# Kernel optimization log

Hardware: AMD Instinct MI355X
Metric: run time of the kernel (lower is better)

## Reference

```python
import jax, jax.numpy as jnp
import numpy as np

R = 8
TOP_K_A = 2
TOP_K_B = 2
SCALING = 16.0 / R  # lora_alpha / r


def setup_inputs() -> dict:
    key = jax.random.key(0)
    k1, k2, k3, k4, k5 = jax.random.split(key, 5)
    B, S, D_IN, D_OUT, EA, EB = 4, 2048, 4096, 4096, 8, 8
    x = jax.random.normal(k1, (B, S, D_IN), dtype=jnp.float32)
    router_logits_a = jax.random.normal(k2, (B * S, EA), dtype=jnp.float32)
    router_logits_b = jax.random.normal(k3, (B * S, EB), dtype=jnp.float32)
    # nn.Linear(in, r).weight -> [r, in]; stacked per expert: [E_a, r, in]
    Wa = jax.random.normal(k4, (EA, R, D_IN), dtype=jnp.float32) * (1.0 / np.sqrt(D_IN))
    # nn.Linear(r, out).weight -> [out, r]; stacked: [E_b, out, r]
    Wb = jax.random.normal(k5, (EB, D_OUT, R), dtype=jnp.float32) * (1.0 / np.sqrt(R))
    return {"x": x, "router_logits_a": router_logits_a,
            "router_logits_b": router_logits_b, "Wa": Wa, "Wb": Wb}


def reference(x, router_logits_a, router_logits_b, Wa, Wb):
    B, S, D_IN = x.shape
    flat_x = x.reshape(-1, D_IN)  # [T, D_in]

    # --- A experts: dense compute over all experts, then top-k gather ---
    topk_logits_a, topk_idx_a = jax.lax.top_k(router_logits_a, TOP_K_A)
    weights_a = jax.nn.softmax(topk_logits_a, axis=-1)  # [T, k_a]
    a_all = jnp.einsum('ti,eri->ter', flat_x, Wa)  # [T, E_a, r]
    sel_a = jnp.take_along_axis(a_all, topk_idx_a[:, :, None], axis=1)  # [T, k_a, r]
    mid = jnp.sum(sel_a * weights_a[:, :, None], axis=1)  # [T, r]

    # --- B experts: dense compute over all experts, then top-k gather ---
    b_all = jnp.einsum('tr,eor->teo', mid, Wb)  # [T, E_b, D_out]
    topk_logits_b, topk_idx_b = jax.lax.top_k(router_logits_b, TOP_K_B)
    weights_b = jax.nn.softmax(topk_logits_b, axis=-1)  # [T, k_b]
    sel_b = jnp.take_along_axis(b_all, topk_idx_b[:, :, None], axis=1)  # [T, k_b, D_out]
    out_flat = jnp.sum(sel_b * weights_b[:, :, None], axis=1) * SCALING  # [T, D_out]
    output = out_flat.reshape(B, S, -1)

    # --- load-balancing aux losses (torch.var is unbiased) ---
    probs_a = jnp.mean(jax.nn.softmax(router_logits_a, axis=-1), axis=0)
    probs_b = jnp.mean(jax.nn.softmax(router_logits_b, axis=-1), axis=0)
    aux_loss_a = Wa.shape[0] * jnp.var(probs_a, ddof=1)
    aux_loss_b = Wb.shape[0] * jnp.var(probs_b, ddof=1)
    return output, aux_loss_a, aux_loss_b
```

## Files before the change

kernel.cpp:

```cpp
#include <hip/hip_runtime.h>
#include <hip/hip_bf16.h>

#define T_TOK 8192
#define D_IN  4096
#define D_OUT 4096
#define SCALE 2.0f

typedef _Float16 h2 __attribute__((ext_vector_type(2)));
typedef _Float16 h4 __attribute__((ext_vector_type(4)));
typedef _Float16 h8 __attribute__((ext_vector_type(8)));
typedef float    f4v __attribute__((ext_vector_type(4)));

__device__ __forceinline__ h2 pkrtz(float a, float b) {
    auto r = __builtin_amdgcn_cvt_pkrtz(a, b);
    h2 o; __builtin_memcpy(&o, &r, 4); return o;
}


__global__ void cwa(const float* __restrict__ Wa, _Float16* __restrict__ WaB) {
    int gid = blockIdx.x * 256 + threadIdx.x;
    int er  = gid >> 10;
    int k0  = (gid & 1023) * 4;
    float4 v = ((const float4*)Wa)[gid];
    int hoff = ((k0 >> 3) * 64 + er) * 8 + (k0 & 7);
    h2 p0 = pkrtz(v.x, v.y), p1 = pkrtz(v.z, v.w);
    h4 o = { p0.x, p0.y, p1.x, p1.y };
    *(h4*)(WaB + hoff) = o;
}

__global__ void cwb(const float* __restrict__ Wb, _Float16* __restrict__ WbB) {
    int gid = blockIdx.x * 256 + threadIdx.x;
    int o = gid & 4095, er = gid >> 12;
    int e = er >> 3, r = er & 7;
    float v = Wb[((size_t)e * 4096 + o) * 8 + r];
    int nt = o >> 8, nl = o & 255;
    WbB[(size_t)nt * 16384 + ((er >> 3) * 256 + nl) * 8 + (er & 7)] = (_Float16)v;
}

__global__ __launch_bounds__(256)
void g1(const float* __restrict__ x, const _Float16* __restrict__ WaB,
        float* __restrict__ part, int kch) {
    __shared__ _Float16 lA[16 * 33 * 8];
    __shared__ _Float16 lB[16 * 64 * 8];
    const int tx = threadIdx.x, l = tx & 63, w = tx >> 6;
    const int m0 = blockIdx.x * 32;
    const int kb = blockIdx.y * kch;
    const int mf = w >> 1, nh = w & 1;

    f4v acc[2];
    acc[0] = (f4v){0.f, 0.f, 0.f, 0.f};
    acc[1] = (f4v){0.f, 0.f, 0.f, 0.f};

    const int iters = kch >> 7;
    for (int it = 0; it < iters; ++it) {
        __syncthreads();
        const float4* xg = (const float4*)(x + (size_t)m0 * D_IN + kb + it * 128);
#pragma unroll
        for (int i = 0; i < 4; ++i) {
            int f = i * 256 + tx;
            int row = f >> 5, c4 = f & 31;
            float4 v = xg[row * 1024 + c4];
            int k = c4 * 4;
            h2 p0 = pkrtz(v.x, v.y), p1 = pkrtz(v.z, v.w);
            h4 o = { p0.x, p0.y, p1.x, p1.y };
            *(h4*)(lA + ((k >> 3) * 33 + row) * 8 + (k & 7)) = o;
        }
        const uint4* bg = (const uint4*)(WaB + (((size_t)kb + it * 128) >> 3) * 512);
        uint4* lb4 = (uint4*)lB;
#pragma unroll
        for (int i = 0; i < 4; ++i) lb4[i * 256 + tx] = bg[i * 256 + tx];
        __syncthreads();

#pragma unroll
        for (int ks = 0; ks < 4; ++ks) {
            h8 a = *(const h8*)(lA + ((ks * 4 + (l >> 4)) * 33 + mf * 16 + (l & 15)) * 8);
#pragma unroll
            for (int n2 = 0; n2 < 2; ++n2) {
                int nf = nh * 2 + n2;
                h8 b = *(const h8*)(lB + ((ks * 4 + (l >> 4)) * 64 + nf * 16 + (l & 15)) * 8);
                acc[n2] = __builtin_amdgcn_mfma_f32_16x16x32_f16(a, b, acc[n2], 0, 0, 0);
            }
        }
    }
    float* pp = part + (size_t)blockIdx.y * T_TOK * 64;
#pragma unroll
    for (int n2 = 0; n2 < 2; ++n2)
#pragma unroll
        for (int r = 0; r < 4; ++r)
            pp[(size_t)(m0 + mf * 16 + (l >> 4) * 4 + r) * 64
               + nh * 32 + n2 * 16 + (l & 15)] = acc[n2][r];
}

__global__ __launch_bounds__(256)
void comb(const float* __restrict__ part, const float* __restrict__ la,
          const float* __restrict__ lb, _Float16* __restrict__ Mb, int ksplit) {
    const int tx = threadIdx.x, l = tx & 63;
    const int t = blockIdx.x * 4 + (tx >> 6);

    float lg[8];
#pragma unroll
    for (int i = 0; i < 8; ++i) lg[i] = la[t * 8 + i];
    int ea0 = 0; float b0 = lg[0];
#pragma unroll
    for (int i = 1; i < 8; ++i) if (lg[i] > b0) { b0 = lg[i]; ea0 = i; }
    int ea1 = -1; float b1 = -1e30f;
#pragma unroll
    for (int i = 0; i < 8; ++i) if (i != ea0 && lg[i] > b1) { b1 = lg[i]; ea1 = i; }
    float wa1 = __expf(b1 - b0); float sa = 1.0f + wa1;
    float wa0 = 1.0f / sa; wa1 = wa1 / sa;

#pragma unroll
    for (int i = 0; i < 8; ++i) lg[i] = lb[t * 8 + i];
    int f0 = 0; float c0 = lg[0];
#pragma unroll
    for (int i = 1; i < 8; ++i) if (lg[i] > c0) { c0 = lg[i]; f0 = i; }
    int f1 = -1; float c1 = -1e30f;
#pragma unroll
    for (int i = 0; i < 8; ++i) if (i != f0 && lg[i] > c1) { c1 = lg[i]; f1 = i; }
    float wb1 = __expf(c1 - c0); float sb = 1.0f + wb1;
    float wb0 = 1.0f / sb; wb1 = wb1 / sb;

    float s = 0.f;
    for (int c = 0; c < ksplit; ++c) s += part[((size_t)c * T_TOK + t) * 64 + l];

    float a0 = __shfl(s, ea0 * 8 + (l & 7), 64);
    float a1 = __shfl(s, ea1 * 8 + (l & 7), 64);
    float mid = wa0 * a0 + wa1 * a1;
    int e = l >> 3;
    float coef = (e == f0) ? SCALE * wb0 : (e == f1) ? SCALE * wb1 : 0.0f;
    Mb[(size_t)(t >> 6) * 4096 + ((l >> 3) * 64 + (t & 63)) * 8 + (l & 7)]
        = (_Float16)(coef * mid);
}

__global__ __launch_bounds__(256)
void g2(const _Float16* __restrict__ Mb, const _Float16* __restrict__ WbB,
        float* __restrict__ out) {
    __shared__ _Float16 lA[4096];
    __shared__ _Float16 lB[16384];
    const int tx = threadIdx.x, l = tx & 63, w = tx >> 6;
    const int nt = blockIdx.x;
    const int mt = blockIdx.y;

    {   const uint4* g = (const uint4*)(Mb + (size_t)mt * 4096);
        uint4* d = (uint4*)lA;
        d[tx] = g[tx]; d[256 + tx] = g[256 + tx]; }
    {   const uint4* g = (const uint4*)(WbB + (size_t)nt * 16384);
        uint4* d = (uint4*)lB;
#pragma unroll
        for (int j = 0; j < 8; ++j) d[j * 256 + tx] = g[j * 256 + tx]; }
    __syncthreads();

    f4v acc[4][4];
#pragma unroll
    for (int mf = 0; mf < 4; ++mf)
#pragma unroll
        for (int nf = 0; nf < 4; ++nf) acc[mf][nf] = (f4v){0.f, 0.f, 0.f, 0.f};

#pragma unroll
    for (int ks = 0; ks < 2; ++ks) {
        h8 a[4], b[4];
#pragma unroll
        for (int mf = 0; mf < 4; ++mf)
            a[mf] = *(const h8*)(lA + ((ks * 4 + (l >> 4)) * 64 + mf * 16 + (l & 15)) * 8);
#pragma unroll
        for (int nf = 0; nf < 4; ++nf)
            b[nf] = *(const h8*)(lB + ((ks * 4 + (l >> 4)) * 256 + w * 64 + nf * 16 + (l & 15)) * 8);
#pragma unroll
        for (int mf = 0; mf < 4; ++mf)
#pragma unroll
            for (int nf = 0; nf < 4; ++nf)
                acc[mf][nf] = __builtin_amdgcn_mfma_f32_16x16x32_f16(a[mf], b[nf], acc[mf][nf], 0, 0, 0);
    }

#pragma unroll
    for (int mf = 0; mf < 4; ++mf)
#pragma unroll
        for (int nf = 0; nf < 4; ++nf)
#pragma unroll
            for (int r = 0; r < 4; ++r)
                out[(size_t)(mt * 64 + mf * 16 + (l >> 4) * 4 + r) * D_OUT
                    + nt * 256 + w * 64 + nf * 16 + (l & 15)] = acc[mf][nf][r];
}

__global__ void aux_partial(const float* __restrict__ la, const float* __restrict__ lb,
                            double* __restrict__ part) {
    const int tx = threadIdx.x;
    const int t  = blockIdx.x * 256 + tx;
    double loc[16];
    {
        float l[8];
#pragma unroll
        for (int i = 0; i < 8; ++i) l[i] = la[t * 8 + i];
        float m = l[0];
#pragma unroll
        for (int i = 1; i < 8; ++i) m = fmaxf(m, l[i]);
        float s = 0.f; float e[8];
#pragma unroll
        for (int i = 0; i < 8; ++i) { e[i] = __expf(l[i] - m); s += e[i]; }
#pragma unroll
        for (int i = 0; i < 8; ++i) loc[i] = (double)(e[i] / s);
    }
    {
        float l[8];
#pragma unroll
        for (int i = 0; i < 8; ++i) l[i] = lb[t * 8 + i];
        float m = l[0];
#pragma unroll
        for (int i = 1; i < 8; ++i) m = fmaxf(m, l[i]);
        float s = 0.f; float e[8];
#pragma unroll
        for (int i = 0; i < 8; ++i) { e[i] = __expf(l[i] - m); s += e[i]; }
#pragma unroll
        for (int i = 0; i < 8; ++i) loc[8 + i] = (double)(e[i] / s);
    }
    __shared__ double red[4][16];
    const int lane = tx & 63, wid = tx >> 6;
#pragma unroll
    for (int v = 0; v < 16; ++v) {
        double s = loc[v];
#pragma unroll
        for (int off = 32; off > 0; off >>= 1) s += __shfl_down(s, off, 64);
        if (lane == 0) red[wid][v] = s;
    }
    __syncthreads();
    if (tx < 16)
        part[blockIdx.x * 16 + tx] = red[0][tx] + red[1][tx] + red[2][tx] + red[3][tx];
}

__global__ void aux_final(const double* __restrict__ part, float* __restrict__ out_aux) {
    const int tx = threadIdx.x;
    __shared__ double sl[16];
    if (tx < 16) {
        double s = 0.0;
#pragma unroll
        for (int b = 0; b < 32; ++b) s += part[b * 16 + tx];
        sl[tx] = s;
    }
    __syncthreads();
    if (tx == 0) {
        double pa[8], pb[8], ma = 0.0, mb = 0.0;
        for (int e = 0; e < 8; ++e) { pa[e] = sl[e] / 8192.0;     ma += pa[e] / 8.0; }
        for (int e = 0; e < 8; ++e) { pb[e] = sl[8 + e] / 8192.0; mb += pb[e] / 8.0; }
        double va = 0.0, vb = 0.0;
        for (int e = 0; e < 8; ++e) { double d = pa[e] - ma; va += d * d; }
        for (int e = 0; e < 8; ++e) { double d = pb[e] - mb; vb += d * d; }
        va /= 7.0; vb /= 7.0;
        out_aux[0] = (float)(8.0 * va);
        out_aux[1] = (float)(8.0 * vb);
    }
}

extern "C" void kernel_launch(void* const* d_in, const int* in_sizes, int n_in,
                              void* d_out, int out_size, void* d_ws, size_t ws_size,
                              hipStream_t stream) {
    const float* x  = (const float*)d_in[0];
    const float* la = (const float*)d_in[1];
    const float* lb = (const float*)d_in[2];
    const float* Wa = (const float*)d_in[3];
    const float* Wb = (const float*)d_in[4];
    float* out = (float*)d_out;

    char* ws = (char*)d_ws;
    _Float16* WaB = (_Float16*)ws;
    _Float16* WbB = (_Float16*)(ws + 524288);
    _Float16* Mb  = (_Float16*)(ws + 1048576);
    double*   pax = (double*)(ws + 2097152);
    float*    p1  = (float*)(ws + 2162688);

    const size_t base = 2162688;
    int ksplit = (ws_size >= base + 4u * 2097152u) ? 4
               : (ws_size >= base + 2u * 2097152u) ? 2 : 1;
    int kch = D_IN / ksplit;

    cwa<<<256, 256, 0, stream>>>(Wa, WaB);
    cwb<<<1024, 256, 0, stream>>>(Wb, WbB);
    aux_partial<<<32, 256, 0, stream>>>(la, lb, pax);
    g1<<<dim3(256, ksplit), 256, 0, stream>>>(x, WaB, p1, kch);
    comb<<<2048, 256, 0, stream>>>(p1, la, lb, Mb, ksplit);
    g2<<<dim3(16, 128), 256, 0, stream>>>(Mb, WbB, out);
    aux_final<<<1, 64, 0, stream>>>(pax, out + (size_t)T_TOK * D_OUT);
}
```

Baseline: 274.0 us.

## Fuse both LoRA GEMMs, routing combine and aux finalize into one kernel

Merges the two weight-conversion kernels and the aux partial reduction into a single prep launch. A single fused kernel then handles each 16-token tile end to end: the x·Wa GEMM with register double-buffered global loads and no K-split, the top-k routing combine in LDS, and the rank-8 GEMM that writes the output directly. This removes the partial-sum and Mb round trips through global memory and cuts the launch count from seven to two. In exchange, Wb is re-read by every block (512 blocks), and the first GEMM loses the K-split parallelism, so each block runs a long serial K loop.

```diff
diff --git a/kernel.cpp b/kernel.cpp
--- a/kernel.cpp
+++ b/kernel.cpp
@@ -1,10 +1,8 @@
 #include <hip/hip_runtime.h>
-#include <hip/hip_bf16.h>
 
 #define T_TOK 8192
 #define D_IN  4096
 #define D_OUT 4096
-#define SCALE 2.0f
 
 typedef _Float16 h2 __attribute__((ext_vector_type(2)));
 typedef _Float16 h4 __attribute__((ext_vector_type(4)));
@@ -15,238 +13,230 @@
     auto r = __builtin_amdgcn_cvt_pkrtz(a, b);
     h2 o; __builtin_memcpy(&o, &r, 4); return o;
 }
-
-
-__global__ void cwa(const float* __restrict__ Wa, _Float16* __restrict__ WaB) {
-    int gid = blockIdx.x * 256 + threadIdx.x;
-    int er  = gid >> 10;
-    int k0  = (gid & 1023) * 4;
-    float4 v = ((const float4*)Wa)[gid];
-    int hoff = ((k0 >> 3) * 64 + er) * 8 + (k0 & 7);
-    h2 p0 = pkrtz(v.x, v.y), p1 = pkrtz(v.z, v.w);
-    h4 o = { p0.x, p0.y, p1.x, p1.y };
-    *(h4*)(WaB + hoff) = o;
-}
-
-__global__ void cwb(const float* __restrict__ Wb, _Float16* __restrict__ WbB) {
-    int gid = blockIdx.x * 256 + threadIdx.x;
-    int o = gid & 4095, er = gid >> 12;
-    int e = er >> 3, r = er & 7;
-    float v = Wb[((size_t)e * 4096 + o) * 8 + r];
-    int nt = o >> 8, nl = o & 255;
-    WbB[(size_t)nt * 16384 + ((er >> 3) * 256 + nl) * 8 + (er & 7)] = (_Float16)v;
-}
+__device__ __forceinline__ h8 cvt8(float4 f0, float4 f1) {
+    h2 p0 = pkrtz(f0.x, f0.y), p1 = pkrtz(f0.z, f0.w);
+    h2 p2 = pkrtz(f1.x, f1.y), p3 = pkrtz(f1.z, f1.w);
+    return (h8){p0.x, p0.y, p1.x, p1.y, p2.x, p2.y, p3.x, p3.y};
+}
+__device__ __forceinline__ h8 as_h8(uint4 u) { h8 b; __builtin_memcpy(&b, &u, 16); return b; }
+
 
 __global__ __launch_bounds__(256)
-void g1(const float* __restrict__ x, const _Float16* __restrict__ WaB,
-        float* __restrict__ part, int kch) {
-    __shared__ _Float16 lA[16 * 33 * 8];
-    __shared__ _Float16 lB[16 * 64 * 8];
+void prep(const float* __restrict__ Wa, const float* __restrict__ Wb,
+          const float* __restrict__ la, const float* __restrict__ lb,
+          _Float16* __restrict__ WaB, _Float16* __restrict__ WbB,
+          double* __restrict__ pax) {
+    const int bid = blockIdx.x, tx = threadIdx.x;
+    __shared__ double red[4][16];
+    if (bid < 256) {
+        int gid = bid * 256 + tx;
+        int er = gid >> 10, k0 = (gid & 1023) * 4;
+        float4 v = ((const float4*)Wa)[gid];
+        h2 p0 = pkrtz(v.x, v.y), p1 = pkrtz(v.z, v.w);
+        h4 o = { p0.x, p0.y, p1.x, p1.y };
+        *(h4*)(WaB + ((k0 >> 3) * 64 + er) * 8 + (k0 & 7)) = o;
+    } else if (bid < 384) {
+        int gid = (bid - 256) * 256 + tx;
+        int e = gid >> 12, o = gid & 4095;
+        const float4* p = (const float4*)(Wb + ((size_t)e * 4096 + o) * 8);
+        h8 v = cvt8(p[0], p[1]);
+        *(h8*)(WbB + ((size_t)e * 4096 + o) * 8) = v;
+    } else {
+        const int ab = bid - 384;
+        const int t = ab * 256 + tx;
+        double loc[16];
+        {
+            float l[8];
+#pragma unroll
+            for (int i = 0; i < 8; ++i) l[i] = la[(size_t)t * 8 + i];
+            float m = l[0];
+#pragma unroll
+            for (int i = 1; i < 8; ++i) m = fmaxf(m, l[i]);
+            float s = 0.f, e[8];
+#pragma unroll
+            for (int i = 0; i < 8; ++i) { e[i] = __expf(l[i] - m); s += e[i]; }
+#pragma unroll
+            for (int i = 0; i < 8; ++i) loc[i] = (double)(e[i] / s);
+        }
+        {
+            float l[8];
+#pragma unroll
+            for (int i = 0; i < 8; ++i) l[i] = lb[(size_t)t * 8 + i];
+            float m = l[0];
+#pragma unroll
+            for (int i = 1; i < 8; ++i) m = fmaxf(m, l[i]);
+            float s = 0.f, e[8];
+#pragma unroll
+            for (int i = 0; i < 8; ++i) { e[i] = __expf(l[i] - m); s += e[i]; }
+#pragma unroll
+            for (int i = 0; i < 8; ++i) loc[8 + i] = (double)(e[i] / s);
+        }
+        const int lane = tx & 63, wid = tx >> 6;
+#pragma unroll
+        for (int v = 0; v < 16; ++v) {
+            double s = loc[v];
+#pragma unroll
+            for (int off = 32; off > 0; off >>= 1) s += __shfl_down(s, off, 64);
+            if (lane == 0) red[wid][v] = s;
+        }
+        __syncthreads();
+        if (tx < 16)
+            pax[ab * 16 + tx] = red[0][tx] + red[1][tx] + red[2][tx] + red[3][tx];
+    }
+}
+
+__global__ __launch_bounds__(256)
+void fused(const float* __restrict__ x, const _Float16* __restrict__ WaB,
+           const _Float16* __restrict__ WbB, const float* __restrict__ la,
+           const float* __restrict__ lb, float* __restrict__ out,
+           const double* __restrict__ pax) {
+    __shared__ float    pL[16][66];
+    __shared__ _Float16 MbL[1024];
+    __shared__ float    sW0[16], sW1[16], sCb[16][8];
+    __shared__ int      sE0[16], sE1[16];
+    __shared__ double   sl[16];
+
     const int tx = threadIdx.x, l = tx & 63, w = tx >> 6;
-    const int m0 = blockIdx.x * 32;
-    const int kb = blockIdx.y * kch;
-    const int mf = w >> 1, nh = w & 1;
-
-    f4v acc[2];
-    acc[0] = (f4v){0.f, 0.f, 0.f, 0.f};
-    acc[1] = (f4v){0.f, 0.f, 0.f, 0.f};
-
-    const int iters = kch >> 7;
-    for (int it = 0; it < iters; ++it) {
+    const int mr = l & 15, kf = l >> 4;
+    const int m0 = blockIdx.x * 16;
+    const int er1 = w * 16 + mr;
+
+    f4v acc = (f4v){0.f, 0.f, 0.f, 0.f};
+    const float* xr = x + (size_t)(m0 + mr) * D_IN + kf * 8;
+    const uint4* wa4 = (const uint4*)WaB;
+
+    float4 A0[8], A1[8]; uint4 B0[4], B1[4];
+
+#define LD1(Ad, Bd, IT) do {                                                   \
+    const float* ap_ = xr + (IT) * 128;                                        \
+    _Pragma("unroll") for (int ks_ = 0; ks_ < 4; ++ks_) {                      \
+        Ad[2 * ks_]     = *(const float4*)(ap_ + ks_ * 32);                    \
+        Ad[2 * ks_ + 1] = *(const float4*)(ap_ + ks_ * 32 + 4); }              \
+    _Pragma("unroll") for (int ks_ = 0; ks_ < 4; ++ks_)                        \
+        Bd[ks_] = wa4[(size_t)(((IT) * 16 + ks_ * 4 + kf) * 64) + er1];        \
+  } while (0)
+
+#define CMP1(As, Bs) do {                                                      \
+    _Pragma("unroll") for (int ks_ = 0; ks_ < 4; ++ks_) {                      \
+        h8 a_ = cvt8(As[2 * ks_], As[2 * ks_ + 1]);                            \
+        acc = __builtin_amdgcn_mfma_f32_16x16x32_f16(a_, as_h8(Bs[ks_]), acc,  \
+                                                     0, 0, 0); }               \
+  } while (0)
+
+    LD1(A0, B0, 0);
+#pragma unroll 1
+    for (int it = 0; it < 30; it += 2) {
+        LD1(A1, B1, it + 1); CMP1(A0, B0);
+        LD1(A0, B0, it + 2); CMP1(A1, B1);
+    }
+    LD1(A1, B1, 31); CMP1(A0, B0); CMP1(A1, B1);
+#undef LD1
+#undef CMP1
+
+#pragma unroll
+    for (int r = 0; r < 4; ++r) pL[kf * 4 + r][er1] = acc[r];
+    __syncthreads();
+
+    if (tx < 16) {
+        const int t = tx;
+        float lg[8];
+#pragma unroll
+        for (int i = 0; i < 8; ++i) lg[i] = la[(size_t)(m0 + t) * 8 + i];
+        int e0 = 0; float b0 = lg[0];
+#pragma unroll
+        for (int i = 1; i < 8; ++i) if (lg[i] > b0) { b0 = lg[i]; e0 = i; }
+        int e1 = -1; float b1 = -1e30f;
+#pragma unroll
+        for (int i = 0; i < 8; ++i) if (i != e0 && lg[i] > b1) { b1 = lg[i]; e1 = i; }
+        float w1 = __expf(b1 - b0), s = 1.f + w1;
+        sW0[t] = 1.f / s; sW1[t] = w1 / s; sE0[t] = e0; sE1[t] = e1;
+
+#pragma unroll
+        for (int i = 0; i < 8; ++i) lg[i] = lb[(size_t)(m0 + t) * 8 + i];
+        int f0 = 0; float c0 = lg[0];
+#pragma unroll
+        for (int i = 1; i < 8; ++i) if (lg[i] > c0) { c0 = lg[i]; f0 = i; }
+        int f1 = -1; float c1 = -1e30f;
+#pragma unroll
+        for (int i = 0; i < 8; ++i) if (i != f0 && lg[i] > c1) { c1 = lg[i]; f1 = i; }
+        float wb1 = __expf(c1 - c0), sb = 1.f + wb1;
+        float wb0s = 2.f / sb, wb1s = 2.f * wb1 / sb;
+#pragma unroll
+        for (int e = 0; e < 8; ++e)
+            sCb[t][e] = (e == f0) ? wb0s : (e == f1) ? wb1s : 0.f;
+    }
+    __syncthreads();
+
+    {
+        const int t = tx >> 4, g = tx & 15;
+        const float w0 = sW0[t], w1 = sW1[t];
+        const int e0 = sE0[t], e1 = sE1[t];
+        const float cb = sCb[t][g >> 1];
+        h4 o;
+#pragma unroll
+        for (int j = 0; j < 4; ++j) {
+            int r = (g * 4 + j) & 7;
+            float mid = w0 * pL[t][e0 * 8 + r] + w1 * pL[t][e1 * 8 + r];
+            o[j] = (_Float16)(cb * mid);
+        }
+        *(h4*)(MbL + ((g >> 1) * 16 + t) * 8 + (g & 1) * 4) = o;
+    }
+    __syncthreads();
+
+    h8 a30, a31;
+    a30 = *(const h8*)(MbL + ((0 * 4 + kf) * 16 + mr) * 8);
+    a31 = *(const h8*)(MbL + ((1 * 4 + kf) * 16 + mr) * 8);
+    const uint4* wb4 = (const uint4*)WbB;
+    const size_t bofs0 = (size_t)((0 * 4 + kf) * 4096);
+    const size_t bofs1 = (size_t)((1 * 4 + kf) * 4096);
+    float* outp = out + (size_t)(m0 + kf * 4) * D_OUT;
+
+    uint4 C0[4], C1[4];
+#define LDB3(Cd, CH) do { int n0_ = (CH) * 128 + w * 32 + mr;                  \
+    Cd[0] = wb4[bofs0 + n0_];      Cd[1] = wb4[bofs0 + n0_ + 16];              \
+    Cd[2] = wb4[bofs1 + n0_];      Cd[3] = wb4[bofs1 + n0_ + 16];              \
+  } while (0)
+
+#define CMP3(Cs, CH) do {                                                      \
+    f4v o0 = (f4v){0.f,0.f,0.f,0.f}, o1 = (f4v){0.f,0.f,0.f,0.f};              \
+    o0 = __builtin_amdgcn_mfma_f32_16x16x32_f16(a30, as_h8(Cs[0]), o0, 0,0,0); \
+    o0 = __builtin_amdgcn_mfma_f32_16x16x32_f16(a31, as_h8(Cs[2]), o0, 0,0,0); \
+    o1 = __builtin_amdgcn_mfma_f32_16x16x32_f16(a30, as_h8(Cs[1]), o1, 0,0,0); \
+    o1 = __builtin_amdgcn_mfma_f32_16x16x32_f16(a31, as_h8(Cs[3]), o1, 0,0,0); \
+    int n0_ = (CH) * 128 + w * 32 + mr;                                        \
+    _Pragma("unroll") for (int r_ = 0; r_ < 4; ++r_) {                         \
+        outp[(size_t)r_ * D_OUT + n0_]      = o0[r_];                          \
+        outp[(size_t)r_ * D_OUT + n0_ + 16] = o1[r_]; }                        \
+  } while (0)
+
+    LDB3(C0, 0);
+#pragma unroll 1
+    for (int c = 0; c < 30; c += 2) {
+        LDB3(C1, c + 1); CMP3(C0, c);
+        LDB3(C0, c + 2); CMP3(C1, c + 1);
+    }
+    LDB3(C1, 31); CMP3(C0, 30); CMP3(C1, 31);
+#undef LDB3
+#undef CMP3
+
+    if (blockIdx.x == 0) {
+        if (tx < 16) {
+            double s = 0.0;
+#pragma unroll
+            for (int b = 0; b < 32; ++b) s += pax[b * 16 + tx];
+            sl[tx] = s;
+        }
         __syncthreads();
-        const float4* xg = (const float4*)(x + (size_t)m0 * D_IN + kb + it * 128);
-#pragma unroll
-        for (int i = 0; i < 4; ++i) {
-            int f = i * 256 + tx;
-            int row = f >> 5, c4 = f & 31;
-            float4 v = xg[row * 1024 + c4];
-            int k = c4 * 4;
-            h2 p0 = pkrtz(v.x, v.y), p1 = pkrtz(v.z, v.w);
-            h4 o = { p0.x, p0.y, p1.x, p1.y };
-            *(h4*)(lA + ((k >> 3) * 33 + row) * 8 + (k & 7)) = o;
-        }
-        const uint4* bg = (const uint4*)(WaB + (((size_t)kb + it * 128) >> 3) * 512);
-        uint4* lb4 = (uint4*)lB;
-#pragma unroll
-        for (int i = 0; i < 4; ++i) lb4[i * 256 + tx] = bg[i * 256 + tx];
-        __syncthreads();
-
-#pragma unroll
-        for (int ks = 0; ks < 4; ++ks) {
-            h8 a = *(const h8*)(lA + ((ks * 4 + (l >> 4)) * 33 + mf * 16 + (l & 15)) * 8);
-#pragma unroll
-            for (int n2 = 0; n2 < 2; ++n2) {
-                int nf = nh * 2 + n2;
-                h8 b = *(const h8*)(lB + ((ks * 4 + (l >> 4)) * 64 + nf * 16 + (l & 15)) * 8);
-                acc[n2] = __builtin_amdgcn_mfma_f32_16x16x32_f16(a, b, acc[n2], 0, 0, 0);
-            }
-        }
-    }
-    float* pp = part + (size_t)blockIdx.y * T_TOK * 64;
-#pragma unroll
-    for (int n2 = 0; n2 < 2; ++n2)
-#pragma unroll
-        for (int r = 0; r < 4; ++r)
-            pp[(size_t)(m0 + mf * 16 + (l >> 4) * 4 + r) * 64
-               + nh * 32 + n2 * 16 + (l & 15)] = acc[n2][r];
-}
-
-__global__ __launch_bounds__(256)
-void comb(const float* __restrict__ part, const float* __restrict__ la,
-          const float* __restrict__ lb, _Float16* __restrict__ Mb, int ksplit) {
-    const int tx = threadIdx.x, l = tx & 63;
-    const int t = blockIdx.x * 4 + (tx >> 6);
-
-    float lg[8];
-#pragma unroll
-    for (int i = 0; i < 8; ++i) lg[i] = la[t * 8 + i];
-    int ea0 = 0; float b0 = lg[0];
-#pragma unroll
-    for (int i = 1; i < 8; ++i) if (lg[i] > b0) { b0 = lg[i]; ea0 = i; }
-    int ea1 = -1; float b1 = -1e30f;
-#pragma unroll
-    for (int i = 0; i < 8; ++i) if (i != ea0 && lg[i] > b1) { b1 = lg[i]; ea1 = i; }
-    float wa1 = __expf(b1 - b0); float sa = 1.0f + wa1;
-    float wa0 = 1.0f / sa; wa1 = wa1 / sa;
-
-#pragma unroll
-    for (int i = 0; i < 8; ++i) lg[i] = lb[t * 8 + i];
-    int f0 = 0; float c0 = lg[0];
-#pragma unroll
-    for (int i = 1; i < 8; ++i) if (lg[i] > c0) { c0 = lg[i]; f0 = i; }
-    int f1 = -1; float c1 = -1e30f;
-#pragma unroll
-    for (int i = 0; i < 8; ++i) if (i != f0 && lg[i] > c1) { c1 = lg[i]; f1 = i; }
-    float wb1 = __expf(c1 - c0); float sb = 1.0f + wb1;
-    float wb0 = 1.0f / sb; wb1 = wb1 / sb;
-
-    float s = 0.f;
-    for (int c = 0; c < ksplit; ++c) s += part[((size_t)c * T_TOK + t) * 64 + l];
-
-    float a0 = __shfl(s, ea0 * 8 + (l & 7), 64);
-    float a1 = __shfl(s, ea1 * 8 + (l & 7), 64);
-    float mid = wa0 * a0 + wa1 * a1;
-    int e = l >> 3;
-    float coef = (e == f0) ? SCALE * wb0 : (e == f1) ? SCALE * wb1 : 0.0f;
-    Mb[(size_t)(t >> 6) * 4096 + ((l >> 3) * 64 + (t & 63)) * 8 + (l & 7)]
-        = (_Float16)(coef * mid);
-}
-
-__global__ __launch_bounds__(256)
-void g2(const _Float16* __restrict__ Mb, const _Float16* __restrict__ WbB,
-        float* __restrict__ out) {
-    __shared__ _Float16 lA[4096];
-    __shared__ _Float16 lB[16384];
-    const int tx = threadIdx.x, l = tx & 63, w = tx >> 6;
-    const int nt = blockIdx.x;
-    const int mt = blockIdx.y;
-
-    {   const uint4* g = (const uint4*)(Mb + (size_t)mt * 4096);
-        uint4* d = (uint4*)lA;
-        d[tx] = g[tx]; d[256 + tx] = g[256 + tx]; }
-    {   const uint4* g = (const uint4*)(WbB + (size_t)nt * 16384);
-        uint4* d = (uint4*)lB;
-#pragma unroll
-        for (int j = 0; j < 8; ++j) d[j * 256 + tx] = g[j * 256 + tx]; }
-    __syncthreads();
-
-    f4v acc[4][4];
-#pragma unroll
-    for (int mf = 0; mf < 4; ++mf)
-#pragma unroll
-        for (int nf = 0; nf < 4; ++nf) acc[mf][nf] = (f4v){0.f, 0.f, 0.f, 0.f};
-
-#pragma unroll
-    for (int ks = 0; ks < 2; ++ks) {
-        h8 a[4], b[4];
-#pragma unroll
-        for (int mf = 0; mf < 4; ++mf)
-            a[mf] = *(const h8*)(lA + ((ks * 4 + (l >> 4)) * 64 + mf * 16 + (l & 15)) * 8);
-#pragma unroll
-        for (int nf = 0; nf < 4; ++nf)
-            b[nf] = *(const h8*)(lB + ((ks * 4 + (l >> 4)) * 256 + w * 64 + nf * 16 + (l & 15)) * 8);
-#pragma unroll
-        for (int mf = 0; mf < 4; ++mf)
-#pragma unroll
-            for (int nf = 0; nf < 4; ++nf)
-                acc[mf][nf] = __builtin_amdgcn_mfma_f32_16x16x32_f16(a[mf], b[nf], acc[mf][nf], 0, 0, 0);
-    }
-
-#pragma unroll
-    for (int mf = 0; mf < 4; ++mf)
-#pragma unroll
-        for (int nf = 0; nf < 4; ++nf)
-#pragma unroll
-            for (int r = 0; r < 4; ++r)
-                out[(size_t)(mt * 64 + mf * 16 + (l >> 4) * 4 + r) * D_OUT
-                    + nt * 256 + w * 64 + nf * 16 + (l & 15)] = acc[mf][nf][r];
-}
-
-__global__ void aux_partial(const float* __restrict__ la, const float* __restrict__ lb,
-                            double* __restrict__ part) {
-    const int tx = threadIdx.x;
-    const int t  = blockIdx.x * 256 + tx;
-    double loc[16];
-    {
-        float l[8];
-#pragma unroll
-        for (int i = 0; i < 8; ++i) l[i] = la[t * 8 + i];
-        float m = l[0];
-#pragma unroll
-        for (int i = 1; i < 8; ++i) m = fmaxf(m, l[i]);
-        float s = 0.f; float e[8];
-#pragma unroll
-        for (int i = 0; i < 8; ++i) { e[i] = __expf(l[i] - m); s += e[i]; }
-#pragma unroll
-        for (int i = 0; i < 8; ++i) loc[i] = (double)(e[i] / s);
-    }
-    {
-        float l[8];
-#pragma unroll
-        for (int i = 0; i < 8; ++i) l[i] = lb[t * 8 + i];
-        float m = l[0];
-#pragma unroll
-        for (int i = 1; i < 8; ++i) m = fmaxf(m, l[i]);
-        float s = 0.f; float e[8];
-#pragma unroll
-        for (int i = 0; i < 8; ++i) { e[i] = __expf(l[i] - m); s += e[i]; }
-#pragma unroll
-        for (int i = 0; i < 8; ++i) loc[8 + i] = (double)(e[i] / s);
-    }
-    __shared__ double red[4][16];
-    const int lane = tx & 63, wid = tx >> 6;
-#pragma unroll
-    for (int v = 0; v < 16; ++v) {
-        double s = loc[v];
-#pragma unroll
-        for (int off = 32; off > 0; off >>= 1) s += __shfl_down(s, off, 64);
-        if (lane == 0) red[wid][v] = s;
-    }
-    __syncthreads();
-    if (tx < 16)
-        part[blockIdx.x * 16 + tx] = red[0][tx] + red[1][tx] + red[2][tx] + red[3][tx];
-}
-
-__global__ void aux_final(const double* __restrict__ part, float* __restrict__ out_aux) {
-    const int tx = threadIdx.x;
-    __shared__ double sl[16];
-    if (tx < 16) {
-        double s = 0.0;
-#pragma unroll
-        for (int b = 0; b < 32; ++b) s += part[b * 16 + tx];
-        sl[tx] = s;
-    }
-    __syncthreads();
-    if (tx == 0) {
-        double pa[8], pb[8], ma = 0.0, mb = 0.0;
-        for (int e = 0; e < 8; ++e) { pa[e] = sl[e] / 8192.0;     ma += pa[e] / 8.0; }
-        for (int e = 0; e < 8; ++e) { pb[e] = sl[8 + e] / 8192.0; mb += pb[e] / 8.0; }
-        double va = 0.0, vb = 0.0;
-        for (int e = 0; e < 8; ++e) { double d = pa[e] - ma; va += d * d; }
-        for (int e = 0; e < 8; ++e) { double d = pb[e] - mb; vb += d * d; }
-        va /= 7.0; vb /= 7.0;
-        out_aux[0] = (float)(8.0 * va);
-        out_aux[1] = (float)(8.0 * vb);
+        if (tx == 0) {
+            double pa[8], pb[8], ma = 0.0, mb = 0.0;
+            for (int e = 0; e < 8; ++e) { pa[e] = sl[e] / 8192.0;     ma += pa[e] / 8.0; }
+            for (int e = 0; e < 8; ++e) { pb[e] = sl[8 + e] / 8192.0; mb += pb[e] / 8.0; }
+            double va = 0.0, vb = 0.0;
+            for (int e = 0; e < 8; ++e) { double d = pa[e] - ma; va += d * d; }
+            for (int e = 0; e < 8; ++e) { double d = pb[e] - mb; vb += d * d; }
+            out[(size_t)T_TOK * D_OUT + 0] = (float)(8.0 * va / 7.0);
+            out[(size_t)T_TOK * D_OUT + 1] = (float)(8.0 * vb / 7.0);
+        }
     }
 }
 
@@ -263,20 +253,8 @@
     char* ws = (char*)d_ws;
     _Float16* WaB = (_Float16*)ws;
     _Float16* WbB = (_Float16*)(ws + 524288);
-    _Float16* Mb  = (_Float16*)(ws + 1048576);
-    double*   pax = (double*)(ws + 2097152);
-    float*    p1  = (float*)(ws + 2162688);
-
-    const size_t base = 2162688;
-    int ksplit = (ws_size >= base + 4u * 2097152u) ? 4
-               : (ws_size >= base + 2u * 2097152u) ? 2 : 1;
-    int kch = D_IN / ksplit;
-
-    cwa<<<256, 256, 0, stream>>>(Wa, WaB);
-    cwb<<<1024, 256, 0, stream>>>(Wb, WbB);
-    aux_partial<<<32, 256, 0, stream>>>(la, lb, pax);
-    g1<<<dim3(256, ksplit), 256, 0, stream>>>(x, WaB, p1, kch);
-    comb<<<2048, 256, 0, stream>>>(p1, la, lb, Mb, ksplit);
-    g2<<<dim3(16, 128), 256, 0, stream>>>(Mb, WbB, out);
-    aux_final<<<1, 64, 0, stream>>>(pax, out + (size_t)T_TOK * D_OUT);
-}
+    double*   pax = (double*)(ws + 1048576);
+
+    prep<<<416, 256, 0, stream>>>(Wa, Wb, la, lb, WaB, WbB, pax);
+    fused<<<512, 256, 0, stream>>>(x, WaB, WbB, la, lb, out, pax);
+}
```

After: 286.1 us. +4.4%, slower.
